# Kernel optimization log

Hardware: AMD Instinct MI355X
Metric: run time of the kernel (lower is better)

## Reference

```python
import jax, jax.numpy as jnp
import numpy as np

NUM_CENTROIDS = 64
NUM_KMEANS = 5
KM_ITERS = 20


def _kmeans_labels(X, key):
    """Lloyd k-means on X [N,D]; returns final cluster labels [N] (int32).
    Mirrors faiss.Kmeans(dim, num_centroids, niter=...) label assignment."""
    N, D = X.shape
    idx = jax.random.choice(key, N, (NUM_CENTROIDS,), replace=False)
    cent0 = X[idx]  # [C,D] init from random data points

    def assign(cent):
        d = (cent * cent).sum(-1)[None, :] - 2.0 * (X @ cent.T)  # [N,C]
        return jnp.argmin(d, axis=1)

    def step(cent, _):
        lab = assign(cent)
        sums = jax.ops.segment_sum(X, lab, num_segments=NUM_CENTROIDS)  # [C,D]
        cnts = jax.ops.segment_sum(jnp.ones((N,), X.dtype), lab, num_segments=NUM_CENTROIDS)
        newc = jnp.where(cnts[:, None] > 0, sums / jnp.maximum(cnts, 1.0)[:, None], cent)
        return newc, None

    cent, _ = jax.lax.scan(step, cent0, None, length=KM_ITERS)
    return assign(cent)


def setup_inputs() -> dict:
    key = jax.random.key(0)
    k1, k2, k3 = jax.random.split(key, 3)
    N, D = 8192, 512
    adj = jax.random.uniform(k1, (N, N), dtype=jnp.float32)
    student = jax.random.normal(k2, (N, D), dtype=jnp.float32)
    teacher = jax.random.normal(k3, (N, D), dtype=jnp.float32)
    return {"adj": adj, "student": student, "teacher": teacher, "topk": 16}


def reference(adj, student, teacher, topk):
    N, D = student.shape
    # similarity = (student @ teacher.T).detach() + 10*I
    sim = jax.lax.stop_gradient(student @ teacher.T) + 10.0 * jnp.eye(N, dtype=student.dtype)
    _, I_knn = jax.lax.top_k(sim, topk)  # [N, k], sorted descending
    rows = jnp.arange(N)[:, None]  # [N,1]

    # knn_neighbor: sparse ones at (row, I_knn); topk cols are distinct per row
    knn_pat = jnp.zeros((N, N), adj.dtype).at[rows, I_knn].set(1.0)
    locality = knn_pat * adj  # sparse elementwise product knn_neighbor * adj

    # k-means cluster labels over NUM_KMEANS seeds (teacher is detached/cpu in torch)
    Xt = jax.lax.stop_gradient(teacher)
    keys = jax.random.split(jax.random.key(1234), NUM_KMEANS)
    labels = jax.vmap(lambda k: _kmeans_labels(Xt, k))(keys)  # [M,N]

    # close-in-background mask: any seed where label(i) == label(knn_j(i))
    ngh_lab = labels[:, I_knn]               # [M,N,k]
    mask = jnp.any(labels[:, :, None] == ngh_lab, axis=0)  # [N,k]

    # globality: ones at masked (row, knn) positions
    glob_pat = jnp.zeros((N, N), adj.dtype).at[rows, I_knn].add(mask.astype(adj.dtype))

    # pos = locality + globality (dense equivalent of coalesced sparse sum)
    pos = locality + glob_pat
    return pos
```

## Files before the change

kernel.cpp:

```cpp
#include <hip/hip_runtime.h>
#include <stdint.h>

typedef unsigned int u32;
typedef unsigned long long u64;
typedef __attribute__((ext_vector_type(8))) short short8;
typedef __attribute__((ext_vector_type(4))) float f32x4;

#define NN 8192
#define DD 512
#define CC 64
#define RR 5
#define KM_ITERS 20
#define TOPKK 16
#define CHUNK 1024
#define GAP_TH 0.05f
#define FLAGTH 0.02f
#define BAND_TH 0.01f

#define MFMA_BF16 __builtin_amdgcn_mfma_f32_16x16x32_bf16

__device__ __forceinline__ void gload16(void* lds, const void* g) {
  __builtin_amdgcn_global_load_lds(
      (const __attribute__((address_space(1))) void*)g,
      (__attribute__((address_space(3))) void*)lds, 16, 0, 0);
}

__device__ __forceinline__ void tf2x32(u32 k0, u32 k1, u32 x0, u32 x1,
                                       u32& o0, u32& o1) {
  u32 ks2 = k0 ^ k1 ^ 0x1BD11BDAu;
  x0 += k0; x1 += k1;
#define TFR(r) { x0 += x1; x1 = (x1 << r) | (x1 >> (32 - r)); x1 ^= x0; }
  TFR(13) TFR(15) TFR(26) TFR(6)
  x0 += k1; x1 += ks2 + 1u;
  TFR(17) TFR(29) TFR(16) TFR(24)
  x0 += ks2; x1 += k0 + 2u;
  TFR(13) TFR(15) TFR(26) TFR(6)
  x0 += k0; x1 += k1 + 3u;
  TFR(17) TFR(29) TFR(16) TFR(24)
  x0 += k1; x1 += ks2 + 4u;
  TFR(13) TFR(15) TFR(26) TFR(6)
  x0 += ks2; x1 += k0 + 5u;
#undef TFR
  o0 = x0; o1 = x1;
}

__global__ __launch_bounds__(256) void rng_kernel(u32* __restrict__ bits1,
                                                  u32* __restrict__ bits2) {
  int r = blockIdx.x;
  int i = blockIdx.y * 256 + threadIdx.x;
  u32 rk0, rk1; tf2x32(0u, 1234u, 0u, (u32)r, rk0, rk1);
  u32 k10, k11, s10, s11, s20, s21;
  tf2x32(rk0, rk1, 0u, 0u, k10, k11);
  tf2x32(rk0, rk1, 0u, 1u, s10, s11);
  tf2x32(k10, k11, 0u, 1u, s20, s21);
  u32 a, b;
  tf2x32(s10, s11, 0u, (u32)i, a, b);
  bits1[r * NN + i] = a ^ b;
  tf2x32(s20, s21, 0u, (u32)i, a, b);
  bits2[r * NN + i] = a ^ b;
}

__global__ __launch_bounds__(256) void rankpart_kernel(const u32* __restrict__ bits,
                                                       u32* __restrict__ prank) {
  __shared__ u64 sk[2048];
  int r = blockIdx.x, zc = blockIdx.z;
  const u32* bb = bits + (size_t)r * NN;
  int jbase = zc * 2048;
  for (int t = threadIdx.x; t < 2048; t += 256)
    sk[t] = ((u64)bb[jbase + t] << 13) | (u32)(jbase + t);
  __syncthreads();
  int i = blockIdx.y * 256 + threadIdx.x;
  u64 ki = ((u64)bb[i] << 13) | (u32)i;
  int cnt = 0;
#pragma unroll 8
  for (int j = 0; j < 2048; ++j) cnt += (int)(sk[j] < ki);
  prank[(size_t)(r * 4 + zc) * NN + i] = cnt;
}

__global__ __launch_bounds__(256) void scat1_kernel(const u32* __restrict__ prank,
                                                    int* __restrict__ vout) {
  int r = blockIdx.x;
  int i = blockIdx.y * 256 + threadIdx.x;
  int rank = prank[(size_t)(r * 4 + 0) * NN + i] + prank[(size_t)(r * 4 + 1) * NN + i] +
             prank[(size_t)(r * 4 + 2) * NN + i] + prank[(size_t)(r * 4 + 3) * NN + i];
  vout[(size_t)r * NN + rank] = i;
}

__global__ __launch_bounds__(256) void scat2_kernel(const u32* __restrict__ prank,
                                                    const int* __restrict__ v1,
                                                    int* __restrict__ sel) {
  int r = blockIdx.x;
  int i = blockIdx.y * 256 + threadIdx.x;
  int rank = prank[(size_t)(r * 4 + 0) * NN + i] + prank[(size_t)(r * 4 + 1) * NN + i] +
             prank[(size_t)(r * 4 + 2) * NN + i] + prank[(size_t)(r * 4 + 3) * NN + i];
  if (rank < CC) sel[r * CC + rank] = v1[(size_t)r * NN + i];
}

__device__ __forceinline__ double block_reduce_d(double s, double* red4) {
  int tid = threadIdx.x;
  for (int off = 32; off > 0; off >>= 1) s += __shfl_down(s, off, 64);
  if ((tid & 63) == 0) red4[tid >> 6] = s;
  __syncthreads();
  return red4[0] + red4[1] + red4[2] + red4[3];
}

__device__ __forceinline__ u32 bf16rne(float a) {
  u32 ab = __float_as_uint(a);
  return (ab + 0x7FFFu + ((ab >> 16) & 1u)) >> 16;
}
__device__ __forceinline__ void splitf(float a, unsigned short& hi, unsigned short& lo) {
  u32 h = bf16rne(a);
  float hf = __uint_as_float(h << 16);
  hi = (unsigned short)h;
  lo = (unsigned short)bf16rne(a - hf);
}

__global__ __launch_bounds__(256) void init_cent_kernel(const float* __restrict__ X,
                                                        const int* __restrict__ sel,
                                                        double* __restrict__ centD,
                                                        double* __restrict__ cnD,
                                                        float* __restrict__ cnF,
                                                        unsigned short* __restrict__ CHg,
                                                        unsigned short* __restrict__ CLg) {
  __shared__ double red4[4];
  int r = blockIdx.x, c = blockIdx.y, t = threadIdx.x;
  int src = sel[r * CC + c];
  const float* xp = X + (size_t)src * DD;
  size_t o = (size_t)(r * CC + c) * DD;
  double va = (double)xp[t], vb = (double)xp[t + 256];
  centD[o + t] = va; centD[o + t + 256] = vb;
  unsigned short h0, l0, h1, l1;
  splitf((float)va, h0, l0); splitf((float)vb, h1, l1);
  CHg[o + t] = h0; CLg[o + t] = l0;
  CHg[o + t + 256] = h1; CLg[o + t + 256] = l1;
  double tot = block_reduce_d(va * va + vb * vb, red4);
  if (t == 0) { cnD[r * CC + c] = tot; cnF[r * CC + c] = (float)tot; }
}

__global__ __launch_bounds__(256) void split_kernel(const float* __restrict__ in,
                                                    unsigned short* __restrict__ hi,
                                                    unsigned short* __restrict__ lo) {
  size_t base = ((size_t)blockIdx.x * 256 + threadIdx.x) * 8;
  float4 v0 = *(const float4*)(in + base);
  float4 v1 = *(const float4*)(in + base + 4);
  float vv[8] = {v0.x, v0.y, v0.z, v0.w, v1.x, v1.y, v1.z, v1.w};
  unsigned short h[8], l[8];
#pragma unroll
  for (int j = 0; j < 8; ++j) splitf(vv[j], h[j], l[j]);
  uint4 hv, lv;
  hv.x = h[0] | ((u32)h[1] << 16); hv.y = h[2] | ((u32)h[3] << 16);
  hv.z = h[4] | ((u32)h[5] << 16); hv.w = h[6] | ((u32)h[7] << 16);
  lv.x = l[0] | ((u32)l[1] << 16); lv.y = l[2] | ((u32)l[3] << 16);
  lv.z = l[4] | ((u32)l[5] << 16); lv.w = l[6] | ((u32)l[7] << 16);
  *(uint4*)(hi + base) = hv;
  *(uint4*)(lo + base) = lv;
}

__global__ __launch_bounds__(256) void assign_kernel(const unsigned short* __restrict__ XH,
                                                     const unsigned short* __restrict__ XL,
                                                     const unsigned short* __restrict__ CHg,
                                                     const unsigned short* __restrict__ CLg,
                                                     const float* __restrict__ cnF,
                                                     const float* __restrict__ Xf,
                                                     const double* __restrict__ centD,
                                                     const double* __restrict__ cnD,
                                                     int* __restrict__ labels,
                                                     int* __restrict__ bhist,
                                                     int* __restrict__ rib) {
  __shared__ unsigned short Xh[64 * 32], Xl[64 * 32], Ch[64 * 32], Cl[64 * 32];
  __shared__ float dmat[64 * 68];
  __shared__ int labs[64];
  __shared__ int flagged[64];
  __shared__ int nflag;
  __shared__ double darr[CC];
  __shared__ int h[CC];
  int r = blockIdx.y;
  int blk = blockIdx.x;
  int rowBase = blk * 64;
  int tid = threadIdx.x;
  int wid = tid >> 6, lane = tid & 63, m = lane & 15, q = lane >> 4;
  int srow = wid * 16 + (lane >> 2);
  int sslot = (lane & 3) * 8;
  const unsigned short* gxh = XH + (size_t)(rowBase + srow) * DD + sslot;
  const unsigned short* gxl = XL + (size_t)(rowBase + srow) * DD + sslot;
  const unsigned short* gch = CHg + ((size_t)r * CC + srow) * DD + sslot;
  const unsigned short* gcl = CLg + ((size_t)r * CC + srow) * DD + sslot;
  unsigned short* dXh = &Xh[wid * 512];
  unsigned short* dXl = &Xl[wid * 512];
  unsigned short* dCh = &Ch[wid * 512];
  unsigned short* dCl = &Cl[wid * 512];
  f32x4 acc[4] = {};
  for (int kc = 0; kc < DD; kc += 32) {
    gload16(dXh, gxh + kc);
    gload16(dXl, gxl + kc);
    gload16(dCh, gch + kc);
    gload16(dCl, gcl + kc);
    __syncthreads();
    short8 ah = *(short8*)&Xh[(wid * 16 + m) * 32 + q * 8];
    short8 al = *(short8*)&Xl[(wid * 16 + m) * 32 + q * 8];
#pragma unroll
    for (int nt = 0; nt < 4; ++nt) {
      short8 bh = *(short8*)&Ch[(nt * 16 + m) * 32 + q * 8];
      short8 bl = *(short8*)&Cl[(nt * 16 + m) * 32 + q * 8];
      acc[nt] = MFMA_BF16(ah, bh, acc[nt], 0, 0, 0);
      acc[nt] = MFMA_BF16(ah, bl, acc[nt], 0, 0, 0);
      acc[nt] = MFMA_BF16(al, bh, acc[nt], 0, 0, 0);
    }
    __syncthreads();
  }
#pragma unroll
  for (int nt = 0; nt < 4; ++nt) {
    float cn = cnF[r * CC + nt * 16 + m];
#pragma unroll
    for (int reg = 0; reg < 4; ++reg)
      dmat[(wid * 16 + q * 4 + reg) * 68 + nt * 16 + m] = cn - 2.0f * acc[nt][reg];
  }
  if (tid == 0) nflag = 0;
  if (tid < CC) h[tid] = 0;
  __syncthreads();
  if (tid < 64) {
    const float* dr = dmat + (size_t)tid * 68;
    float best = dr[0], second = 3.4e38f; int bi = 0;
    for (int c = 1; c < CC; ++c) {
      float v = dr[c];
      if (v < best) { second = best; best = v; bi = c; }
      else if (v < second) second = v;
    }
    labs[tid] = bi;
    if (second - best < GAP_TH) {
      int s = atomicAdd(&nflag, 1);
      flagged[s] = tid;
    }
  }
  __syncthreads();
  int nf = nflag;
  int cc0 = tid >> 2, sub = tid & 3;
  for (int f = 0; f < nf; ++f) {
    int row = flagged[f];
    const float* x = Xf + (size_t)(rowBase + row) * DD + sub * 128;
    const double* cp = centD + (size_t)(r * CC + cc0) * DD + sub * 128;
    double s = 0.0;
    for (int k = 0; k < 128; ++k) s += (double)x[k] * cp[k];
    s += __shfl_down(s, 2, 64);
    s += __shfl_down(s, 1, 64);
    if (sub == 0) darr[cc0] = cnD[r * CC + cc0] - 2.0 * s;
    __syncthreads();
    if (tid == 0) {
      double best = darr[0]; int bi = 0;
      for (int c2 = 1; c2 < CC; ++c2) { double v = darr[c2]; if (v < best) { best = v; bi = c2; } }
      labs[row] = bi;
    }
    __syncthreads();
  }
  if (tid < 64) {
    int lab = labs[tid];
    atomicAdd(&h[lab], 1);
    int rk = 0;
    for (int j = 0; j < tid; ++j) rk += (labs[j] == lab);
    rib[(size_t)r * NN + rowBase + tid] = rk;
    labels[(size_t)r * NN + rowBase + tid] = lab;
  }
  __syncthreads();
  if (tid < CC) bhist[(size_t)(r * 128 + blk) * CC + tid] = h[tid];
}

__global__ __launch_bounds__(256) void fill_kernel(const int* __restrict__ labels,
                                                   const int* __restrict__ rib,
                                                   const int* __restrict__ bhist,
                                                   int* __restrict__ cstart,
                                                   int* __restrict__ cnt,
                                                   int* __restrict__ member) {
  __shared__ int bh[128 * CC];
  __shared__ int cs[CC];
  __shared__ int tots[CC];
  int r = blockIdx.x, blk = blockIdx.y, tid = threadIdx.x;
  const int* src = bhist + (size_t)r * 128 * CC;
  for (int t = tid; t < 128 * CC; t += 256) bh[t] = src[t];
  __syncthreads();
  if (tid < CC) {
    int run = 0;
    for (int b = 0; b < 128; ++b) { int v = bh[b * CC + tid]; bh[b * CC + tid] = run; run += v; }
    tots[tid] = run;
  }
  __syncthreads();
  if (tid == 0) {
    int run = 0;
    for (int q2 = 0; q2 < CC; ++q2) { cs[q2] = run; run += tots[q2]; }
  }
  __syncthreads();
  int i = blk * 256 + tid;
  int lab = labels[(size_t)r * NN + i];
  int pos = cs[lab] + bh[(i >> 6) * CC + lab] + rib[(size_t)r * NN + i];
  member[(size_t)r * NN + pos] = i;
  if (blk == 0 && tid < CC) { cnt[r * CC + tid] = tots[tid]; cstart[r * CC + tid] = cs[tid]; }
}

__global__ __launch_bounds__(256) void update_kernel(const float* __restrict__ X,
                                                     const int* __restrict__ member,
                                                     const int* __restrict__ cstart,
                                                     const int* __restrict__ cnt,
                                                     const double* __restrict__ centOld,
                                                     double* __restrict__ centNew) {
  __shared__ double part[4][64];
  int r = blockIdx.x, c = blockIdx.y, dchunk = blockIdx.z;
  int tid = threadIdx.x;
  int d = dchunk * 64 + (tid & 63);
  int lane = tid >> 6;
  int n = cnt[r * CC + c];
  int st = cstart[r * CC + c];
  const int* mem = member + (size_t)r * NN + st;
  int n4 = (n + 3) >> 2;
  int lo = lane * n4;
  int hi = min(n, lo + n4);
  double s0 = 0, s1 = 0, s2 = 0, s3 = 0;
  int m = lo;
  for (; m + 3 < hi; m += 4) {
    s0 += (double)X[(size_t)mem[m + 0] * DD + d];
    s1 += (double)X[(size_t)mem[m + 1] * DD + d];
    s2 += (double)X[(size_t)mem[m + 2] * DD + d];
    s3 += (double)X[(size_t)mem[m + 3] * DD + d];
  }
  for (; m < hi; ++m) s0 += (double)X[(size_t)mem[m] * DD + d];
  part[lane][tid & 63] = (s0 + s1) + (s2 + s3);
  __syncthreads();
  if (tid < 64) {
    double tot = (part[0][tid] + part[1][tid]) + (part[2][tid] + part[3][tid]);
    size_t o = (size_t)(r * CC + c) * DD + dchunk * 64 + tid;
    double va = (n > 0) ? tot / (double)n : centOld[o];
    centNew[o] = va;
  }
}

__global__ __launch_bounds__(256) void norm_kernel(const double* __restrict__ centNew,
                                                   double* __restrict__ cnD,
                                                   float* __restrict__ cnF,
                                                   unsigned short* __restrict__ CHg,
                                                   unsigned short* __restrict__ CLg) {
  __shared__ double red4[4];
  int r = blockIdx.x, c = blockIdx.y, t = threadIdx.x;
  size_t o = (size_t)(r * CC + c) * DD;
  double va = centNew[o + t], vb = centNew[o + t + 256];
  unsigned short h0, l0, h1, l1;
  splitf((float)va, h0, l0); splitf((float)vb, h1, l1);
  CHg[o + t] = h0; CLg[o + t] = l0;
  CHg[o + t + 256] = h1; CLg[o + t + 256] = l1;
  double tot = block_reduce_d(va * va + vb * vb, red4);
  if (t == 0) { cnD[r * CC + c] = tot; cnF[r * CC + c] = (float)tot; }
}

__global__ __launch_bounds__(256) void gemm_kernel(const unsigned short* __restrict__ SH,
                                                   const unsigned short* __restrict__ SL,
                                                   const unsigned short* __restrict__ TH,
                                                   const unsigned short* __restrict__ TL,
                                                   float* __restrict__ sim,
                                                   int rowChunk) {
  __shared__ unsigned short Ah[128 * 32], Al[128 * 32], Bh[128 * 32], Bl[128 * 32];
  int tid = threadIdx.x;
  int wid = tid >> 6, lane = tid & 63, m = lane & 15, q = lane >> 4;
  int waveM = wid >> 1, waveN = wid & 1;
  int rowBase = rowChunk + blockIdx.y * 128;
  int colBase = blockIdx.x * 128;
  int sr0 = wid * 16 + (lane >> 2);
  int sr1 = (wid + 4) * 16 + (lane >> 2);
  int sslot = (lane & 3) * 8;
  const unsigned short* gah0 = SH + (size_t)(rowBase + sr0) * DD + sslot;
  const unsigned short* gah1 = SH + (size_t)(rowBase + sr1) * DD + sslot;
  const unsigned short* gal0 = SL + (size_t)(rowBase + sr0) * DD + sslot;
  const unsigned short* gal1 = SL + (size_t)(rowBase + sr1) * DD + sslot;
  const unsigned short* gbh0 = TH + (size_t)(colBase + sr0) * DD + sslot;
  const unsigned short* gbh1 = TH + (size_t)(colBase + sr1) * DD + sslot;
  const unsigned short* gbl0 = TL + (size_t)(colBase + sr0) * DD + sslot;
  const unsigned short* gbl1 = TL + (size_t)(colBase + sr1) * DD + sslot;
  unsigned short* dA0 = &Ah[wid * 512];       unsigned short* dA1 = &Ah[(wid + 4) * 512];
  unsigned short* dAl0 = &Al[wid * 512];      unsigned short* dAl1 = &Al[(wid + 4) * 512];
  unsigned short* dB0 = &Bh[wid * 512];       unsigned short* dB1 = &Bh[(wid + 4) * 512];
  unsigned short* dBl0 = &Bl[wid * 512];      unsigned short* dBl1 = &Bl[(wid + 4) * 512];
  f32x4 acc[4][4] = {};
  for (int kc = 0; kc < DD; kc += 32) {
    gload16(dA0, gah0 + kc);  gload16(dA1, gah1 + kc);
    gload16(dAl0, gal0 + kc); gload16(dAl1, gal1 + kc);
    gload16(dB0, gbh0 + kc);  gload16(dB1, gbh1 + kc);
    gload16(dBl0, gbl0 + kc); gload16(dBl1, gbl1 + kc);
    __syncthreads();
    short8 ah[4], al[4], bh[4], bl[4];
#pragma unroll
    for (int t = 0; t < 4; ++t) {
      ah[t] = *(short8*)&Ah[(waveM * 64 + t * 16 + m) * 32 + q * 8];
      al[t] = *(short8*)&Al[(waveM * 64 + t * 16 + m) * 32 + q * 8];
      bh[t] = *(short8*)&Bh[(waveN * 64 + t * 16 + m) * 32 + q * 8];
      bl[t] = *(short8*)&Bl[(waveN * 64 + t * 16 + m) * 32 + q * 8];
    }
#pragma unroll
    for (int mt = 0; mt < 4; ++mt)
#pragma unroll
      for (int nt = 0; nt < 4; ++nt) {
        acc[mt][nt] = MFMA_BF16(ah[mt], bh[nt], acc[mt][nt], 0, 0, 0);
        acc[mt][nt] = MFMA_BF16(ah[mt], bl[nt], acc[mt][nt], 0, 0, 0);
        acc[mt][nt] = MFMA_BF16(al[mt], bh[nt], acc[mt][nt], 0, 0, 0);
      }
    __syncthreads();
  }
#pragma unroll
  for (int mt = 0; mt < 4; ++mt)
#pragma unroll
    for (int nt = 0; nt < 4; ++nt) {
      int gcol = colBase + waveN * 64 + nt * 16 + m;
#pragma unroll
      for (int reg = 0; reg < 4; ++reg) {
        int lrow = blockIdx.y * 128 + waveM * 64 + mt * 16 + q * 4 + reg;
        int grow = rowChunk + lrow;
        float v = acc[mt][nt][reg];
        if (grow == gcol) v += 10.0f;
        sim[(size_t)lrow * NN + gcol] = v;
      }
    }
}

__global__ __launch_bounds__(256) void topk_kernel(const float* __restrict__ sim,
                                                   const float* __restrict__ S,
                                                   const float* __restrict__ T,
                                                   int* __restrict__ iknn,
                                                   int rowChunk) {
  __shared__ u32 rowk[NN];
  __shared__ int bins[4096];
  __shared__ int partial[256];
  __shared__ u64 cand[128];
  __shared__ u64 sure[40];
  __shared__ u64 outk[TOPKK + 1];
  __shared__ u64 red[4];
  __shared__ int nsure, ncand, selB1, selB2, needSel, hardcase;
  __shared__ int nsureR, nbandR;
  __shared__ int sidx[16];
  __shared__ int bidx[64];
  __shared__ double bval[64];

  int blk = blockIdx.x, tid = threadIdx.x;
  int grow = rowChunk + blk;
  const float* rp = sim + (size_t)blk * NN;

  for (int t = tid; t < 4096; t += 256) bins[t] = 0;
  if (tid == 0) { nsure = 0; ncand = 0; hardcase = 0; }
  __syncthreads();
  for (int t = tid; t < NN; t += 256) {
    u32 u = __float_as_uint(rp[t]);
    u = (u & 0x80000000u) ? ~u : (u | 0x80000000u);
    rowk[t] = u;
    atomicAdd(&bins[u >> 20], 1);
  }
  __syncthreads();
  int ps = 0;
#pragma unroll
  for (int b = 0; b < 16; ++b) ps += bins[tid * 16 + b];
  partial[tid] = ps;
  __syncthreads();
  if (tid == 0) {
    int cum = 0, c = 255;
    for (; c > 0; --c) { if (cum + partial[c] >= 17) break; cum += partial[c]; }
    int b = c * 16 + 15;
    for (; b > c * 16; --b) { if (cum + bins[b] >= 17) break; cum += bins[b]; }
    selB1 = b; needSel = 17 - cum;
  }
  __syncthreads();
  int B1 = selB1;
  for (int t = tid; t < NN; t += 256) {
    u32 u = rowk[t];
    int b = (int)(u >> 20);
    if (b < B1) continue;
    u64 key = ((u64)u << 32) | (u32)(NN - 1 - t);
    if (b > B1) { int s = atomicAdd(&nsure, 1); if (s < 40) sure[s] = key; else hardcase = 1; }
    else        { int s = atomicAdd(&ncand, 1); if (s < 128) cand[s] = key; }
  }
  __syncthreads();
  if (ncand > 128) {
    for (int t = tid; t < 4096; t += 256) bins[t] = 0;
    __syncthreads();
    for (int t = tid; t < NN; t += 256) {
      u32 u = rowk[t];
      if ((int)(u >> 20) == B1) atomicAdd(&bins[(u >> 8) & 0xFFFu], 1);
    }
    __syncthreads();
    int p2 = 0;
#pragma unroll
    for (int b = 0; b < 16; ++b) p2 += bins[tid * 16 + b];
    partial[tid] = p2;
    __syncthreads();
    if (tid == 0) {
      int need = needSel;
      int cum = 0, c = 255;
      for (; c > 0; --c) { if (cum + partial[c] >= need) break; cum += partial[c]; }
      int b = c * 16 + 15;
      for (; b > c * 16; --b) { if (cum + bins[b] >= need) break; cum += bins[b]; }
      selB2 = b; ncand = 0;
    }
    __syncthreads();
    int B2 = selB2;
    for (int t = tid; t < NN; t += 256) {
      u32 u = rowk[t];
      if ((int)(u >> 20) != B1) continue;
      int sb = (int)((u >> 8) & 0xFFFu);
      if (sb < B2) continue;
      u64 key = ((u64)u << 32) | (u32)(NN - 1 - t);
      if (sb > B2) { int s = atomicAdd(&nsure, 1); if (s < 40) sure[s] = key; else hardcase = 1; }
      else         { int s = atomicAdd(&ncand, 1); if (s < 128) cand[s] = key; }
    }
    __syncthreads();
    if (tid == 0 && ncand > 128) hardcase = 1;
    __syncthreads();
  }
  if (!hardcase) {
    int ns = nsure, nc = ncand;
    int total = ns + nc;
    if (tid < total) {
      u64 k = tid < ns ? sure[tid] : cand[tid - ns];
      int rank = 0;
      for (int j = 0; j < total; ++j) {
        u64 o = j < ns ? sure[j] : cand[j - ns];
        rank += (int)(o > k);
      }
      if (rank < TOPKK + 1) outk[rank] = k;
    }
  } else {
    for (int k = 0; k < TOPKK + 1; ++k) {
      u64 best = 0;
      for (int t = tid; t < NN; t += 256) {
        u64 key = ((u64)rowk[t] << 32) | (u32)(NN - 1 - t);
        best = key > best ? key : best;
      }
      for (int off = 32; off > 0; off >>= 1) {
        u32 lo = (u32)best, hi = (u32)(best >> 32);
        lo = __shfl_down(lo, off, 64); hi = __shfl_down(hi, off, 64);
        u64 o = ((u64)hi << 32) | lo;
        best = o > best ? o : best;
      }
      if ((tid & 63) == 0) red[tid >> 6] = best;
      __syncthreads();
      if (tid == 0) {
        u64 b = red[0];
        for (int w = 1; w < 4; ++w) b = red[w] > b ? red[w] : b;
        outk[k] = b;
        rowk[(NN - 1) - (int)(b & 0xFFFFFFFFu)] = 0;
      }
      __syncthreads();
    }
  }
  __syncthreads();
  if (hardcase && tid < TOPKK + 1) {
    u64 k = outk[tid];
    rowk[(NN - 1) - (int)(k & 0xFFFFFFFFu)] = (u32)(k >> 32);
  }
  __syncthreads();
  if (tid < TOPKK)
    iknn[(size_t)grow * TOPKK + tid] = (NN - 1) - (int)(outk[tid] & 0xFFFFFFFFu);
  u32 ub16 = (u32)(outk[TOPKK - 1] >> 32), ub17 = (u32)(outk[TOPKK] >> 32);
  float v16 = (ub16 & 0x80000000u) ? __uint_as_float(ub16 & 0x7FFFFFFFu)
                                   : __uint_as_float(~ub16);
  float v17 = (ub17 & 0x80000000u) ? __uint_as_float(ub17 & 0x7FFFFFFFu)
                                   : __uint_as_float(~ub17);
  if (v16 - v17 >= FLAGTH) return;

  if (tid == 0) { nsureR = 0; nbandR = 0; }
  __syncthreads();
  for (int j = tid; j < NN; j += 256) {
    u32 u = rowk[j];
    float v = (u & 0x80000000u) ? __uint_as_float(u & 0x7FFFFFFFu)
                                : __uint_as_float(~u);
    if (v > v16 + BAND_TH) {
      int s = atomicAdd(&nsureR, 1);
      if (s < 16) sidx[s] = j;
    } else if (v >= v16 - BAND_TH) {
      int s = atomicAdd(&nbandR, 1);
      if (s < 64) bidx[s] = j;
    }
  }
  __syncthreads();
  int nb = nbandR > 64 ? 64 : nbandR;
  if (tid < nb) {
    const float* sp = S + (size_t)grow * DD;
    const float* tp = T + (size_t)bidx[tid] * DD;
    double s = 0.0;
    for (int k = 0; k < DD; ++k) s += (double)sp[k] * (double)tp[k];
    bval[tid] = s;
  }
  __syncthreads();
  if (tid == 0) {
    int w = 0;
    int ns = nsureR < 16 ? nsureR : 16;
    for (int i2 = 0; i2 < ns; ++i2) iknn[(size_t)grow * TOPKK + w++] = sidx[i2];
    u64 used = 0;
    while (w < TOPKK) {
      int bj = -1; double bv = 0.0;
      for (int i2 = 0; i2 < nb; ++i2) {
        if (used & (1ull << i2)) continue;
        if (bj < 0 || bval[i2] > bv ||
            (bval[i2] == bv && bidx[i2] < bidx[bj])) { bv = bval[i2]; bj = i2; }
      }
      if (bj < 0) break;
      used |= 1ull << bj;
      iknn[(size_t)grow * TOPKK + w++] = bidx[bj];
    }
  }
}

__global__ __launch_bounds__(256) void zero_kernel(float4* __restrict__ out) {
  size_t i = (size_t)blockIdx.x * 256 + threadIdx.x;
  out[i] = make_float4(0.f, 0.f, 0.f, 0.f);
}

__global__ __launch_bounds__(256) void scatter_kernel(const float* __restrict__ adj,
                                                      const int* __restrict__ iknn,
                                                      const int* __restrict__ labels,
                                                      float* __restrict__ out) {
  int idx = blockIdx.x * 256 + threadIdx.x;
  int i = idx >> 4;
  int col = iknn[idx];
  int m = 0;
#pragma unroll
  for (int r = 0; r < RR; ++r)
    m |= (labels[(size_t)r * NN + i] == labels[(size_t)r * NN + col]);
  size_t o = (size_t)i * NN + col;
  out[o] = adj[o] + (float)m;
}

extern "C" void kernel_launch(void* const* d_in, const int* in_sizes, int n_in,
                              void* d_out, int out_size, void* d_ws, size_t ws_size,
                              hipStream_t stream) {
  (void)in_sizes; (void)n_in; (void)out_size; (void)ws_size;
  const float* adj     = (const float*)d_in[0];
  const float* student = (const float*)d_in[1];
  const float* teacher = (const float*)d_in[2];
  float* out = (float*)d_out;

  char* p = (char*)d_ws;
  auto alloc = [&](size_t bytes) -> void* {
    void* q = (void*)p; p += (bytes + 255) & ~(size_t)255; return q;
  };
  double* centA  = (double*)alloc((size_t)RR * CC * DD * 8);
  double* centB  = (double*)alloc((size_t)RR * CC * DD * 8);
  double* cnD    = (double*)alloc((size_t)RR * CC * 8);
  float*  cnF    = (float*) alloc((size_t)RR * CC * 4);
  u32*    bits1  = (u32*)   alloc((size_t)RR * NN * 4);
  u32*    bits2  = (u32*)   alloc((size_t)RR * NN * 4);
  u32*    prank  = (u32*)   alloc((size_t)RR * 4 * NN * 4);
  int*    v1     = (int*)   alloc((size_t)RR * NN * 4);
  int*    sel    = (int*)   alloc((size_t)RR * CC * 4);
  int*    labels = (int*)   alloc((size_t)RR * NN * 4);
  int*    bhist  = (int*)   alloc((size_t)RR * 128 * CC * 4);
  int*    cstart = (int*)   alloc((size_t)RR * CC * 4);
  int*    cnt    = (int*)   alloc((size_t)RR * CC * 4);
  int*    rib    = (int*)   alloc((size_t)RR * NN * 4);
  int*    member = (int*)   alloc((size_t)RR * NN * 4);
  int*    iknn   = (int*)   alloc((size_t)NN * TOPKK * 4);
  unsigned short* SH = (unsigned short*)alloc((size_t)NN * DD * 2);
  unsigned short* SL = (unsigned short*)alloc((size_t)NN * DD * 2);
  unsigned short* THi = (unsigned short*)alloc((size_t)NN * DD * 2);
  unsigned short* TLo = (unsigned short*)alloc((size_t)NN * DD * 2);
  unsigned short* CHg = (unsigned short*)alloc((size_t)RR * CC * DD * 2);
  unsigned short* CLg = (unsigned short*)alloc((size_t)RR * CC * DD * 2);
  float*  simc   = (float*) alloc((size_t)CHUNK * NN * 4);

  rng_kernel<<<dim3(RR, 32), 256, 0, stream>>>(bits1, bits2);
  rankpart_kernel<<<dim3(RR, 32, 4), 256, 0, stream>>>(bits1, prank);
  scat1_kernel<<<dim3(RR, 32), 256, 0, stream>>>(prank, v1);
  rankpart_kernel<<<dim3(RR, 32, 4), 256, 0, stream>>>(bits2, prank);
  scat2_kernel<<<dim3(RR, 32), 256, 0, stream>>>(prank, v1, sel);
  init_cent_kernel<<<dim3(RR, CC), 256, 0, stream>>>(teacher, sel, centA, cnD, cnF, CHg, CLg);

  split_kernel<<<(NN * DD / 8) / 256, 256, 0, stream>>>(student, SH, SL);
  split_kernel<<<(NN * DD / 8) / 256, 256, 0, stream>>>(teacher, THi, TLo);

  double* cur = centA; double* nxt = centB;
  for (int it = 0; it < KM_ITERS; ++it) {
    assign_kernel<<<dim3(NN / 64, RR), 256, 0, stream>>>(THi, TLo, CHg, CLg, cnF,
                                                         teacher, cur, cnD,
                                                         labels, bhist, rib);
    fill_kernel<<<dim3(RR, 32), 256, 0, stream>>>(labels, rib, bhist, cstart, cnt, member);
    update_kernel<<<dim3(RR, CC, 8), 256, 0, stream>>>(teacher, member, cstart, cnt, cur, nxt);
    norm_kernel<<<dim3(RR, CC), 256, 0, stream>>>(nxt, cnD, cnF, CHg, CLg);
    double* t = cur; cur = nxt; nxt = t;
  }
  assign_kernel<<<dim3(NN / 64, RR), 256, 0, stream>>>(THi, TLo, CHg, CLg, cnF,
                                                       teacher, cur, cnD,
                                                       labels, bhist, rib);

  for (int ch = 0; ch < NN / CHUNK; ++ch) {
    gemm_kernel<<<dim3(NN / 128, CHUNK / 128), 256, 0, stream>>>(SH, SL, THi, TLo, simc,
                                                                 ch * CHUNK);
    topk_kernel<<<CHUNK, 256, 0, stream>>>(simc, student, teacher, iknn, ch * CHUNK);
  }

  zero_kernel<<<(unsigned)((size_t)NN * NN / 4 / 256), 256, 0, stream>>>((float4*)out);
  scatter_kernel<<<NN * TOPKK / 256, 256, 0, stream>>>(adj, iknn, labels, out);
}
```

Baseline: 3.129 ms.

## Double K-step per barrier, swizzle GEMM workgroups, enlarge sim row chunk

Measured after the change: 2.915 ms. -6.8%, faster.

```diff
diff --git a/kernel.cpp b/kernel.cpp
--- a/kernel.cpp
+++ b/kernel.cpp
@@ -12,7 +12,7 @@
 #define RR 5
 #define KM_ITERS 20
 #define TOPKK 16
-#define CHUNK 1024
+#define CHUNK 4096
 #define GAP_TH 0.05f
 #define FLAGTH 0.02f
 #define BAND_TH 0.01f
@@ -167,7 +167,8 @@
                                                      int* __restrict__ labels,
                                                      int* __restrict__ bhist,
                                                      int* __restrict__ rib) {
-  __shared__ unsigned short Xh[64 * 32], Xl[64 * 32], Ch[64 * 32], Cl[64 * 32];
+  __shared__ unsigned short Xh[2 * 64 * 32], Xl[2 * 64 * 32],
+                            Ch[2 * 64 * 32], Cl[2 * 64 * 32];
   __shared__ float dmat[64 * 68];
   __shared__ int labs[64];
   __shared__ int flagged[64];
@@ -185,26 +186,30 @@
   const unsigned short* gxl = XL + (size_t)(rowBase + srow) * DD + sslot;
   const unsigned short* gch = CHg + ((size_t)r * CC + srow) * DD + sslot;
   const unsigned short* gcl = CLg + ((size_t)r * CC + srow) * DD + sslot;
-  unsigned short* dXh = &Xh[wid * 512];
-  unsigned short* dXl = &Xl[wid * 512];
-  unsigned short* dCh = &Ch[wid * 512];
-  unsigned short* dCl = &Cl[wid * 512];
   f32x4 acc[4] = {};
-  for (int kc = 0; kc < DD; kc += 32) {
-    gload16(dXh, gxh + kc);
-    gload16(dXl, gxl + kc);
-    gload16(dCh, gch + kc);
-    gload16(dCl, gcl + kc);
-    __syncthreads();
-    short8 ah = *(short8*)&Xh[(wid * 16 + m) * 32 + q * 8];
-    short8 al = *(short8*)&Xl[(wid * 16 + m) * 32 + q * 8];
-#pragma unroll
-    for (int nt = 0; nt < 4; ++nt) {
-      short8 bh = *(short8*)&Ch[(nt * 16 + m) * 32 + q * 8];
-      short8 bl = *(short8*)&Cl[(nt * 16 + m) * 32 + q * 8];
-      acc[nt] = MFMA_BF16(ah, bh, acc[nt], 0, 0, 0);
-      acc[nt] = MFMA_BF16(ah, bl, acc[nt], 0, 0, 0);
-      acc[nt] = MFMA_BF16(al, bh, acc[nt], 0, 0, 0);
+  for (int kc = 0; kc < DD; kc += 64) {
+#pragma unroll
+    for (int p = 0; p < 2; ++p) {
+      int off = p * 2048, ko = kc + p * 32;
+      gload16(&Xh[off + wid * 512], gxh + ko);
+      gload16(&Xl[off + wid * 512], gxl + ko);
+      gload16(&Ch[off + wid * 512], gch + ko);
+      gload16(&Cl[off + wid * 512], gcl + ko);
+    }
+    __syncthreads();
+#pragma unroll
+    for (int s = 0; s < 2; ++s) {
+      int off = s * 2048;
+      short8 ah = *(short8*)&Xh[off + (wid * 16 + m) * 32 + q * 8];
+      short8 al = *(short8*)&Xl[off + (wid * 16 + m) * 32 + q * 8];
+#pragma unroll
+      for (int nt = 0; nt < 4; ++nt) {
+        short8 bh = *(short8*)&Ch[off + (nt * 16 + m) * 32 + q * 8];
+        short8 bl = *(short8*)&Cl[off + (nt * 16 + m) * 32 + q * 8];
+        acc[nt] = MFMA_BF16(ah, bh, acc[nt], 0, 0, 0);
+        acc[nt] = MFMA_BF16(ah, bl, acc[nt], 0, 0, 0);
+        acc[nt] = MFMA_BF16(al, bh, acc[nt], 0, 0, 0);
+      }
     }
     __syncthreads();
   }
@@ -354,12 +359,18 @@
                                                    const unsigned short* __restrict__ TL,
                                                    float* __restrict__ sim,
                                                    int rowChunk) {
-  __shared__ unsigned short Ah[128 * 32], Al[128 * 32], Bh[128 * 32], Bl[128 * 32];
+  __shared__ unsigned short Ah[2 * 128 * 32], Al[2 * 128 * 32],
+                            Bh[2 * 128 * 32], Bl[2 * 128 * 32];
   int tid = threadIdx.x;
   int wid = tid >> 6, lane = tid & 63, m = lane & 15, q = lane >> 4;
   int waveM = wid >> 1, waveN = wid & 1;
-  int rowBase = rowChunk + blockIdx.y * 128;
-  int colBase = blockIdx.x * 128;
+  const int nwgx = NN / 128;
+  const int nwg = nwgx * (CHUNK / 128);
+  int wg = blockIdx.y * nwgx + blockIdx.x;
+  int swz = (wg & 7) * (nwg >> 3) + (wg >> 3);
+  int rowTile = swz / nwgx, colTile = swz % nwgx;
+  int rowBase = rowChunk + rowTile * 128;
+  int colBase = colTile * 128;
   int sr0 = wid * 16 + (lane >> 2);
   int sr1 = (wid + 4) * 16 + (lane >> 2);
   int sslot = (lane & 3) * 8;
@@ -371,33 +382,41 @@
   const unsigned short* gbh1 = TH + (size_t)(colBase + sr1) * DD + sslot;
   const unsigned short* gbl0 = TL + (size_t)(colBase + sr0) * DD + sslot;
   const unsigned short* gbl1 = TL + (size_t)(colBase + sr1) * DD + sslot;
-  unsigned short* dA0 = &Ah[wid * 512];       unsigned short* dA1 = &Ah[(wid + 4) * 512];
-  unsigned short* dAl0 = &Al[wid * 512];      unsigned short* dAl1 = &Al[(wid + 4) * 512];
-  unsigned short* dB0 = &Bh[wid * 512];       unsigned short* dB1 = &Bh[(wid + 4) * 512];
-  unsigned short* dBl0 = &Bl[wid * 512];      unsigned short* dBl1 = &Bl[(wid + 4) * 512];
   f32x4 acc[4][4] = {};
-  for (int kc = 0; kc < DD; kc += 32) {
-    gload16(dA0, gah0 + kc);  gload16(dA1, gah1 + kc);
-    gload16(dAl0, gal0 + kc); gload16(dAl1, gal1 + kc);
-    gload16(dB0, gbh0 + kc);  gload16(dB1, gbh1 + kc);
-    gload16(dBl0, gbl0 + kc); gload16(dBl1, gbl1 + kc);
-    __syncthreads();
-    short8 ah[4], al[4], bh[4], bl[4];
-#pragma unroll
-    for (int t = 0; t < 4; ++t) {
-      ah[t] = *(short8*)&Ah[(waveM * 64 + t * 16 + m) * 32 + q * 8];
-      al[t] = *(short8*)&Al[(waveM * 64 + t * 16 + m) * 32 + q * 8];
-      bh[t] = *(short8*)&Bh[(waveN * 64 + t * 16 + m) * 32 + q * 8];
-      bl[t] = *(short8*)&Bl[(waveN * 64 + t * 16 + m) * 32 + q * 8];
-    }
-#pragma unroll
-    for (int mt = 0; mt < 4; ++mt)
-#pragma unroll
-      for (int nt = 0; nt < 4; ++nt) {
-        acc[mt][nt] = MFMA_BF16(ah[mt], bh[nt], acc[mt][nt], 0, 0, 0);
-        acc[mt][nt] = MFMA_BF16(ah[mt], bl[nt], acc[mt][nt], 0, 0, 0);
-        acc[mt][nt] = MFMA_BF16(al[mt], bh[nt], acc[mt][nt], 0, 0, 0);
+  for (int kc = 0; kc < DD; kc += 64) {
+#pragma unroll
+    for (int p = 0; p < 2; ++p) {
+      int off = p * 4096, ko = kc + p * 32;
+      gload16(&Ah[off + wid * 512], gah0 + ko);
+      gload16(&Ah[off + (wid + 4) * 512], gah1 + ko);
+      gload16(&Al[off + wid * 512], gal0 + ko);
+      gload16(&Al[off + (wid + 4) * 512], gal1 + ko);
+      gload16(&Bh[off + wid * 512], gbh0 + ko);
+      gload16(&Bh[off + (wid + 4) * 512], gbh1 + ko);
+      gload16(&Bl[off + wid * 512], gbl0 + ko);
+      gload16(&Bl[off + (wid + 4) * 512], gbl1 + ko);
+    }
+    __syncthreads();
+#pragma unroll
+    for (int s = 0; s < 2; ++s) {
+      int off = s * 4096;
+      short8 ah[4], al[4], bh[4], bl[4];
+#pragma unroll
+      for (int t = 0; t < 4; ++t) {
+        ah[t] = *(short8*)&Ah[off + (waveM * 64 + t * 16 + m) * 32 + q * 8];
+        al[t] = *(short8*)&Al[off + (waveM * 64 + t * 16 + m) * 32 + q * 8];
+        bh[t] = *(short8*)&Bh[off + (waveN * 64 + t * 16 + m) * 32 + q * 8];
+        bl[t] = *(short8*)&Bl[off + (waveN * 64 + t * 16 + m) * 32 + q * 8];
       }
+#pragma unroll
+      for (int mt = 0; mt < 4; ++mt)
+#pragma unroll
+        for (int nt = 0; nt < 4; ++nt) {
+          acc[mt][nt] = MFMA_BF16(ah[mt], bh[nt], acc[mt][nt], 0, 0, 0);
+          acc[mt][nt] = MFMA_BF16(ah[mt], bl[nt], acc[mt][nt], 0, 0, 0);
+          acc[mt][nt] = MFMA_BF16(al[mt], bh[nt], acc[mt][nt], 0, 0, 0);
+        }
+    }
     __syncthreads();
   }
 #pragma unroll
@@ -407,7 +426,7 @@
       int gcol = colBase + waveN * 64 + nt * 16 + m;
 #pragma unroll
       for (int reg = 0; reg < 4; ++reg) {
-        int lrow = blockIdx.y * 128 + waveM * 64 + mt * 16 + q * 4 + reg;
+        int lrow = rowTile * 128 + waveM * 64 + mt * 16 + q * 4 + reg;
         int grow = rowChunk + lrow;
         float v = acc[mt][nt][reg];
         if (grow == gcol) v += 10.0f;
```
